# Performance work log

Hardware: AMD Instinct MI355X
Metric: run time of the kernel (lower is better)

## Reference

```python
import jax, jax.numpy as jnp
import numpy as np
import math

EMBED_DIM = 1024
NUM_HEADS = 16
HEAD_DIM = EMBED_DIM // NUM_HEADS
SEQ = 2048
BSZ = 2


def setup_inputs() -> dict:
    key = jax.random.key(0)
    ks = jax.random.split(key, 7)
    # xavier_uniform bound for in_proj_weight [3E, E]
    bound_in = math.sqrt(6.0 / (3 * EMBED_DIM + EMBED_DIM))
    bound_out = math.sqrt(1.0 / EMBED_DIM)  # nn.Linear default kaiming-ish bound
    return {
        "query": jax.random.normal(ks[0], (SEQ, BSZ, EMBED_DIM), dtype=jnp.float32),
        "key": jax.random.normal(ks[1], (SEQ, BSZ, EMBED_DIM), dtype=jnp.float32),
        "value": jax.random.normal(ks[2], (SEQ, BSZ, EMBED_DIM), dtype=jnp.float32),
        "in_proj_weight": jax.random.uniform(ks[3], (3 * EMBED_DIM, EMBED_DIM), minval=-bound_in, maxval=bound_in, dtype=jnp.float32),
        "in_proj_bias": jnp.zeros((3 * EMBED_DIM,), dtype=jnp.float32),
        "out_proj_weight": jax.random.uniform(ks[4], (EMBED_DIM, EMBED_DIM), minval=-bound_out, maxval=bound_out, dtype=jnp.float32),
        "out_proj_bias": jnp.zeros((EMBED_DIM,), dtype=jnp.float32),
    }


def reference(query, key, value, in_proj_weight, in_proj_bias, out_proj_weight, out_proj_bias):
    tgt_len, bsz, embed_dim = query.shape
    src_len = key.shape[0]
    h, d = NUM_HEADS, HEAD_DIM

    w_q, w_k, w_v = jnp.split(in_proj_weight, 3, axis=0)   # each [E, E]
    b_q, b_k, b_v = jnp.split(in_proj_bias, 3, axis=0)     # each [E]

    q = query @ w_q.T + b_q    # [T, B, E]
    k = key @ w_k.T + b_k      # [S, B, E]
    v = value @ w_v.T + b_v    # [S, B, E]

    # [T,B,E] -> [B, H, T, D]
    q = q.reshape(tgt_len, bsz, h, d).transpose(1, 2, 0, 3)
    k = k.reshape(src_len, bsz, h, d).transpose(1, 2, 0, 3)
    v = v.reshape(src_len, bsz, h, d).transpose(1, 2, 0, 3)

    scale = 1.0 / math.sqrt(d)
    scores = jnp.einsum("bhtd,bhsd->bhts", q, k) * scale   # [B, H, T, S]
    attn_probs = jax.nn.softmax(scores, axis=-1)
    out = jnp.einsum("bhts,bhsd->bhtd", attn_probs, v)      # [B, H, T, D]

    # [B,H,T,D] -> [T, B, E]
    out = out.transpose(2, 0, 1, 3).reshape(tgt_len, bsz, embed_dim)
    out = out @ out_proj_weight.T + out_proj_bias
    return (out, attn_probs)
```

## Files before the change

kernel.cpp:

```cpp
#include <hip/hip_runtime.h>


#define LDT 72

typedef __attribute__((ext_vector_type(8))) short short8;
typedef __attribute__((ext_vector_type(4))) float f32x4;

union V16 { float4 f4; unsigned long long u64[2]; unsigned short us[8]; };

__device__ inline unsigned short f2bf(float f) {
  union { float f; unsigned u; } v; v.f = f;
  unsigned u = v.u;
  u += 0x7FFFu + ((u >> 16) & 1u);
  return (unsigned short)(u >> 16);
}

__device__ inline short8 load8(const unsigned short* p) {
  union { short8 v; unsigned long long u[2]; } r;
  r.u[0] = *(const unsigned long long*)(p);
  r.u[1] = *(const unsigned long long*)(p + 4);
  return r.v;
}

__device__ inline void st16(unsigned short* dst, V16 v) {
  *(unsigned long long*)(dst) = v.u64[0];
  *(unsigned long long*)(dst + 4) = v.u64[1];
}

__global__ void cvt_bf16(const float* __restrict__ in, unsigned short* __restrict__ out, int n) {
  int i = (blockIdx.x * 256 + threadIdx.x) * 4;
  if (i < n) {
    float4 f = *(const float4*)(in + i);
    ushort4 o;
    o.x = f2bf(f.x); o.y = f2bf(f.y); o.z = f2bf(f.z); o.w = f2bf(f.w);
    *(ushort4*)(out + i) = o;
  }
}

__global__ __launch_bounds__(256, 2) void gemm_bt(
    const unsigned short* __restrict__ A,
    const unsigned short* __restrict__ Bw,
    const float* __restrict__ bias,
    void* __restrict__ Cv,
    int K, int ldc, int flags)
{
  __shared__ unsigned short As[128 * LDT];
  __shared__ unsigned short Bs[128 * LDT];
  int tid = threadIdx.x;
  int lane = tid & 63;
  int w = tid >> 6;
  int wm = (w & 1) * 64, wn = (w >> 1) * 64;
  int m0 = blockIdx.y * 128, n0 = blockIdx.x * 128;
  int quad = lane >> 4, c = lane & 15;

  f32x4 acc[4][4] = {};

  int lrow = tid >> 1;
  int lk = (tid & 1) * 32;
  const unsigned short* Ap = A + (size_t)(m0 + lrow) * K + lk;
  const unsigned short* Bp = Bw + (size_t)(n0 + lrow) * K + lk;
  unsigned short* AsW = As + lrow * LDT + lk;
  unsigned short* BsW = Bs + lrow * LDT + lk;

  for (int k0 = 0; k0 < K; k0 += 64) {
    V16 a0, a1, a2, a3, b0, b1, b2, b3;
    a0.f4 = *(const float4*)(Ap + k0);
    a1.f4 = *(const float4*)(Ap + k0 + 8);
    a2.f4 = *(const float4*)(Ap + k0 + 16);
    a3.f4 = *(const float4*)(Ap + k0 + 24);
    b0.f4 = *(const float4*)(Bp + k0);
    b1.f4 = *(const float4*)(Bp + k0 + 8);
    b2.f4 = *(const float4*)(Bp + k0 + 16);
    b3.f4 = *(const float4*)(Bp + k0 + 24);
    __syncthreads();
    st16(AsW, a0); st16(AsW + 8, a1); st16(AsW + 16, a2); st16(AsW + 24, a3);
    st16(BsW, b0); st16(BsW + 8, b1); st16(BsW + 16, b2); st16(BsW + 24, b3);
    __syncthreads();

    const unsigned short* Ab = As + (wm + c) * LDT + quad * 8;
    const unsigned short* Bb = Bs + (wn + c) * LDT + quad * 8;
#pragma unroll
    for (int ks = 0; ks < 2; ks++) {
      short8 af[4], bf[4];
#pragma unroll
      for (int i = 0; i < 4; i++) {
        af[i] = load8(Ab + i * 16 * LDT + ks * 32);
        bf[i] = load8(Bb + i * 16 * LDT + ks * 32);
      }
#pragma unroll
      for (int mi = 0; mi < 4; mi++)
#pragma unroll
        for (int ni = 0; ni < 4; ni++)
          acc[mi][ni] = __builtin_amdgcn_mfma_f32_16x16x32_bf16(af[mi], bf[ni], acc[mi][ni], 0, 0, 0);
    }
  }

#pragma unroll
  for (int mi = 0; mi < 4; mi++) {
#pragma unroll
    for (int ni = 0; ni < 4; ni++) {
      int col = n0 + wn + ni * 16 + c;
      float bv = bias[col];
#pragma unroll
      for (int r = 0; r < 4; r++) {
        int row = m0 + wm + mi * 16 + quad * 4 + r;
        float val = acc[mi][ni][r] + bv;
        if (flags & 2) val *= 0.125f;
        if (flags & 1) ((unsigned short*)Cv)[(size_t)row * ldc + col] = f2bf(val);
        else           ((float*)Cv)[(size_t)row * ldc + col] = val;
      }
    }
  }
}

__global__ __launch_bounds__(256, 2) void attn_fused(
    const unsigned short* __restrict__ QKV,
    float* __restrict__ probs,
    unsigned short* __restrict__ attnO)
{
  __shared__ unsigned short Qs[128 * LDT];
  __shared__ unsigned short Ks[64 * LDT];
  __shared__ unsigned short Ps[128 * LDT];
  __shared__ unsigned short Vts[64 * LDT];

  int tid = threadIdx.x, lane = tid & 63, w = tid >> 6;
  int bh = blockIdx.x >> 4;
  int tt = blockIdx.x & 15;
  int b = bh >> 4, h = bh & 15;
  int t0 = tt * 128;
  int quad = lane >> 4, c = lane & 15;
  int rbase = w * 32;

  {
    int row = tid >> 1, lk = (tid & 1) * 32;
    const unsigned short* src = QKV + ((size_t)((t0 + row) * 2 + b)) * 3072 + h * 64 + lk;
    V16 v0, v1, v2, v3;
    v0.f4 = *(const float4*)(src);
    v1.f4 = *(const float4*)(src + 8);
    v2.f4 = *(const float4*)(src + 16);
    v3.f4 = *(const float4*)(src + 24);
    unsigned short* dst = Qs + row * LDT + lk;
    st16(dst, v0); st16(dst + 8, v1); st16(dst + 16, v2); st16(dst + 24, v3);
  }

  int krow = tid >> 2, kseg = (tid & 3) * 16;
  const unsigned short* kbase = QKV + 1024 + h * 64 + kseg;
  const unsigned short* vbase = QKV + 2048 + h * 64 + kseg;
  unsigned short* ksdst = Ks + krow * LDT + kseg;

  float l_part[2][4] = {};

  for (int s0 = 0; s0 < 2048; s0 += 64) {
    V16 v0, v1;
    const unsigned short* src = kbase + ((size_t)((s0 + krow) * 2 + b)) * 3072;
    v0.f4 = *(const float4*)(src);
    v1.f4 = *(const float4*)(src + 8);
    __syncthreads();
    st16(ksdst, v0); st16(ksdst + 8, v1);
    __syncthreads();

    f32x4 sc[2][4] = {};
    const unsigned short* Ab = Qs + (rbase + c) * LDT + quad * 8;
    const unsigned short* Bb = Ks + c * LDT + quad * 8;
#pragma unroll
    for (int ks = 0; ks < 2; ks++) {
      short8 af[2], bfr[4];
      af[0] = load8(Ab + ks * 32);
      af[1] = load8(Ab + 16 * LDT + ks * 32);
#pragma unroll
      for (int ni = 0; ni < 4; ni++) bfr[ni] = load8(Bb + ni * 16 * LDT + ks * 32);
#pragma unroll
      for (int mi = 0; mi < 2; mi++)
#pragma unroll
        for (int ni = 0; ni < 4; ni++)
          sc[mi][ni] = __builtin_amdgcn_mfma_f32_16x16x32_bf16(af[mi], bfr[ni], sc[mi][ni], 0, 0, 0);
    }
#pragma unroll
    for (int mi = 0; mi < 2; mi++)
#pragma unroll
      for (int r = 0; r < 4; r++)
        l_part[mi][r] += __expf(sc[mi][0][r]) + __expf(sc[mi][1][r]) +
                         __expf(sc[mi][2][r]) + __expf(sc[mi][3][r]);
  }

  float rl[2][4];
#pragma unroll
  for (int mi = 0; mi < 2; mi++)
#pragma unroll
    for (int r = 0; r < 4; r++) {
      float s = l_part[mi][r];
      s += __shfl_xor(s, 1); s += __shfl_xor(s, 2);
      s += __shfl_xor(s, 4); s += __shfl_xor(s, 8);
      rl[mi][r] = 1.0f / s;
    }

  f32x4 acc_o[2][4] = {};
  size_t prow_base = ((size_t)bh * 2048 + t0) * 2048;

  for (int s0 = 0; s0 < 2048; s0 += 64) {
    V16 kv0, kv1, vv0, vv1;
    {
      const unsigned short* srcK = kbase + ((size_t)((s0 + krow) * 2 + b)) * 3072;
      kv0.f4 = *(const float4*)(srcK);
      kv1.f4 = *(const float4*)(srcK + 8);
      const unsigned short* srcV = vbase + ((size_t)((s0 + krow) * 2 + b)) * 3072;
      vv0.f4 = *(const float4*)(srcV);
      vv1.f4 = *(const float4*)(srcV + 8);
    }
    __syncthreads();
    st16(ksdst, kv0); st16(ksdst + 8, kv1);
#pragma unroll
    for (int j = 0; j < 8; j++) Vts[(kseg + j) * LDT + krow] = vv0.us[j];
#pragma unroll
    for (int j = 0; j < 8; j++) Vts[(kseg + 8 + j) * LDT + krow] = vv1.us[j];
    __syncthreads();

    f32x4 sc[2][4] = {};
    const unsigned short* Ab = Qs + (rbase + c) * LDT + quad * 8;
    const unsigned short* Bb = Ks + c * LDT + quad * 8;
#pragma unroll
    for (int ks = 0; ks < 2; ks++) {
      short8 af[2], bfr[4];
      af[0] = load8(Ab + ks * 32);
      af[1] = load8(Ab + 16 * LDT + ks * 32);
#pragma unroll
      for (int ni = 0; ni < 4; ni++) bfr[ni] = load8(Bb + ni * 16 * LDT + ks * 32);
#pragma unroll
      for (int mi = 0; mi < 2; mi++)
#pragma unroll
        for (int ni = 0; ni < 4; ni++)
          sc[mi][ni] = __builtin_amdgcn_mfma_f32_16x16x32_bf16(af[mi], bfr[ni], sc[mi][ni], 0, 0, 0);
    }

#pragma unroll
    for (int mi = 0; mi < 2; mi++)
#pragma unroll
      for (int ni = 0; ni < 4; ni++)
#pragma unroll
        for (int r = 0; r < 4; r++) {
          float p = __expf(sc[mi][ni][r]) * rl[mi][r];
          int rloc = rbase + mi * 16 + quad * 4 + r;
          int cloc = ni * 16 + c;
          probs[prow_base + (size_t)rloc * 2048 + s0 + cloc] = p;
          Ps[rloc * LDT + cloc] = f2bf(p);
        }
    __syncthreads();

    const unsigned short* Ab2 = Ps + (rbase + c) * LDT + quad * 8;
    const unsigned short* Bb2 = Vts + c * LDT + quad * 8;
#pragma unroll
    for (int ks = 0; ks < 2; ks++) {
      short8 af[2], bfr[4];
      af[0] = load8(Ab2 + ks * 32);
      af[1] = load8(Ab2 + 16 * LDT + ks * 32);
#pragma unroll
      for (int ni = 0; ni < 4; ni++) bfr[ni] = load8(Bb2 + ni * 16 * LDT + ks * 32);
#pragma unroll
      for (int mi = 0; mi < 2; mi++)
#pragma unroll
        for (int ni = 0; ni < 4; ni++)
          acc_o[mi][ni] = __builtin_amdgcn_mfma_f32_16x16x32_bf16(af[mi], bfr[ni], acc_o[mi][ni], 0, 0, 0);
    }
  }

#pragma unroll
  for (int mi = 0; mi < 2; mi++)
#pragma unroll
    for (int ni = 0; ni < 4; ni++)
#pragma unroll
      for (int r = 0; r < 4; r++) {
        int t = t0 + rbase + mi * 16 + quad * 4 + r;
        attnO[(size_t)(t * 2 + b) * 1024 + h * 64 + ni * 16 + c] = f2bf(acc_o[mi][ni][r]);
      }
}

extern "C" void kernel_launch(void* const* d_in, const int* in_sizes, int n_in,
                              void* d_out, int out_size, void* d_ws, size_t ws_size,
                              hipStream_t stream) {
  (void)in_sizes; (void)n_in; (void)out_size; (void)ws_size;
  const float* q_in  = (const float*)d_in[0];
  const float* k_in  = (const float*)d_in[1];
  const float* v_in  = (const float*)d_in[2];
  const float* w_in  = (const float*)d_in[3];
  const float* b_in  = (const float*)d_in[4];
  const float* w_out = (const float*)d_in[5];
  const float* b_out = (const float*)d_in[6];

  float* out0  = (float*)d_out;
  float* probs = out0 + (size_t)4096 * 1024;

  unsigned short* Xq  = (unsigned short*)d_ws;
  unsigned short* Xk  = Xq + (size_t)4096 * 1024;
  unsigned short* Xv  = Xk + (size_t)4096 * 1024;
  unsigned short* Wi  = Xv + (size_t)4096 * 1024;
  unsigned short* Wo  = Wi + (size_t)3072 * 1024;
  unsigned short* QKV = Wo + (size_t)1024 * 1024;
  unsigned short* AO  = QKV + (size_t)4096 * 3072;

  cvt_bf16<<<4096, 256, 0, stream>>>(q_in, Xq, 4194304);
  cvt_bf16<<<4096, 256, 0, stream>>>(k_in, Xk, 4194304);
  cvt_bf16<<<4096, 256, 0, stream>>>(v_in, Xv, 4194304);
  cvt_bf16<<<3072, 256, 0, stream>>>(w_in, Wi, 3145728);
  cvt_bf16<<<1024, 256, 0, stream>>>(w_out, Wo, 1048576);

  dim3 g1(8, 32);
  gemm_bt<<<g1, 256, 0, stream>>>(Xq, Wi,                       b_in,        QKV,        1024, 3072, 3);
  gemm_bt<<<g1, 256, 0, stream>>>(Xk, Wi + (size_t)1024 * 1024, b_in + 1024, QKV + 1024, 1024, 3072, 1);
  gemm_bt<<<g1, 256, 0, stream>>>(Xv, Wi + (size_t)2048 * 1024, b_in + 2048, QKV + 2048, 1024, 3072, 1);

  attn_fused<<<512, 256, 0, stream>>>(QKV, probs, AO);

  gemm_bt<<<g1, 256, 0, stream>>>(AO, Wo, b_out, (void*)out0, 1024, 1024, 0);
}
```

Baseline: 800.9 us.

## Use direct global-to-LDS loads, double-buffer K/V, pre-transpose V, merge launches

The GEMM and attention kernels now load tiles with global_load_lds into XOR-swizzled, unpadded shared memory. Attention double-buffers the K and V tiles, and V is transposed into a separate buffer by a new kernel so the in-loop scalar LDS transpose goes away. The five conversion launches become one, and the three QKV projections become a single 24x32-block launch. Probability stores switch to nontemporal, and the output projection uses a 64-wide N tile to get more blocks. The goal is lower load latency, fewer bank conflicts and less launch overhead, at the cost of an extra transpose pass and more LDS per block.

Measured after the change: 794.5 us. Within noise of the previous version (-0.8%).

```diff
diff --git a/kernel.cpp b/kernel.cpp
--- a/kernel.cpp
+++ b/kernel.cpp
@@ -8,98 +8,120 @@
 
 union V16 { float4 f4; unsigned long long u64[2]; unsigned short us[8]; };
 
-__device__ inline unsigned short f2bf(float f) {
+__device__ __forceinline__ unsigned short f2bf(float f) {
   union { float f; unsigned u; } v; v.f = f;
   unsigned u = v.u;
   u += 0x7FFFu + ((u >> 16) & 1u);
   return (unsigned short)(u >> 16);
 }
 
-__device__ inline short8 load8(const unsigned short* p) {
+__device__ __forceinline__ short8 load8(const unsigned short* p) {
   union { short8 v; unsigned long long u[2]; } r;
   r.u[0] = *(const unsigned long long*)(p);
   r.u[1] = *(const unsigned long long*)(p + 4);
   return r.v;
 }
 
-__device__ inline void st16(unsigned short* dst, V16 v) {
+__device__ __forceinline__ void st16(unsigned short* dst, V16 v) {
   *(unsigned long long*)(dst) = v.u64[0];
   *(unsigned long long*)(dst + 4) = v.u64[1];
 }
 
-__global__ void cvt_bf16(const float* __restrict__ in, unsigned short* __restrict__ out, int n) {
+typedef const __attribute__((address_space(1))) void* gas_t;
+typedef __attribute__((address_space(3))) void* las_t;
+__device__ __forceinline__ void gld16(const void* g, void* l) {
+  __builtin_amdgcn_global_load_lds((gas_t)g, (las_t)l, 16, 0, 0);
+}
+
+__global__ void cvt_all(const float* __restrict__ q, const float* __restrict__ k,
+                        const float* __restrict__ v, const float* __restrict__ wi,
+                        const float* __restrict__ wo,
+                        unsigned short* __restrict__ oq, unsigned short* __restrict__ ok2,
+                        unsigned short* __restrict__ ov, unsigned short* __restrict__ owi,
+                        unsigned short* __restrict__ owo) {
+  int y = blockIdx.y;
+  const float* src; unsigned short* dst; int n;
+  if (y == 0)      { src = q;  dst = oq;  n = 4194304; }
+  else if (y == 1) { src = k;  dst = ok2; n = 4194304; }
+  else if (y == 2) { src = v;  dst = ov;  n = 4194304; }
+  else if (y == 3) { src = wi; dst = owi; n = 3145728; }
+  else             { src = wo; dst = owo; n = 1048576; }
   int i = (blockIdx.x * 256 + threadIdx.x) * 4;
   if (i < n) {
-    float4 f = *(const float4*)(in + i);
+    float4 f = *(const float4*)(src + i);
     ushort4 o;
     o.x = f2bf(f.x); o.y = f2bf(f.y); o.z = f2bf(f.z); o.w = f2bf(f.w);
-    *(ushort4*)(out + i) = o;
-  }
-}
-
+    *(ushort4*)(dst + i) = o;
+  }
+}
+
+template<int BN>
 __global__ __launch_bounds__(256, 2) void gemm_bt(
-    const unsigned short* __restrict__ A,
-    const unsigned short* __restrict__ Bw,
+    const unsigned short* __restrict__ A0,
+    const unsigned short* __restrict__ A1,
+    const unsigned short* __restrict__ A2,
+    const unsigned short* __restrict__ W,
     const float* __restrict__ bias,
     void* __restrict__ Cv,
-    int K, int ldc, int flags)
+    int K, int ldc, int qkv)
 {
-  __shared__ unsigned short As[128 * LDT];
-  __shared__ unsigned short Bs[128 * LDT];
+  constexpr int NI = BN / 32;
+  __shared__ unsigned short As[128 * 64];
+  __shared__ unsigned short Bs[BN * 64];
   int tid = threadIdx.x;
   int lane = tid & 63;
   int w = tid >> 6;
-  int wm = (w & 1) * 64, wn = (w >> 1) * 64;
-  int m0 = blockIdx.y * 128, n0 = blockIdx.x * 128;
+  int wm = (w & 1) * 64, wn = (w >> 1) * (BN / 2);
+  int m0 = blockIdx.y * 128, n0g = blockIdx.x * BN;
+  int which = qkv ? (n0g >> 10) : 0;
+  const unsigned short* A = (which == 0) ? A0 : ((which == 1) ? A1 : A2);
+  const unsigned short* Bw = W + (size_t)which * (1u << 20);
+  int n0 = qkv ? (n0g & 1023) : n0g;
   int quad = lane >> 4, c = lane & 15;
-
-  f32x4 acc[4][4] = {};
-
-  int lrow = tid >> 1;
-  int lk = (tid & 1) * 32;
-  const unsigned short* Ap = A + (size_t)(m0 + lrow) * K + lk;
-  const unsigned short* Bp = Bw + (size_t)(n0 + lrow) * K + lk;
-  unsigned short* AsW = As + lrow * LDT + lk;
-  unsigned short* BsW = Bs + lrow * LDT + lk;
+  int sw8 = c & 7;
+
+  f32x4 acc[4][NI] = {};
+
+  int srow = lane >> 3;
+  int sseg = ((lane & 7) ^ srow) * 8;
+  const unsigned short* Asrc = A  + (size_t)(m0 + w * 32      + srow) * K + sseg;
+  const unsigned short* Bsrc = Bw + (size_t)(n0 + w * NI * 8  + srow) * K + sseg;
 
   for (int k0 = 0; k0 < K; k0 += 64) {
-    V16 a0, a1, a2, a3, b0, b1, b2, b3;
-    a0.f4 = *(const float4*)(Ap + k0);
-    a1.f4 = *(const float4*)(Ap + k0 + 8);
-    a2.f4 = *(const float4*)(Ap + k0 + 16);
-    a3.f4 = *(const float4*)(Ap + k0 + 24);
-    b0.f4 = *(const float4*)(Bp + k0);
-    b1.f4 = *(const float4*)(Bp + k0 + 8);
-    b2.f4 = *(const float4*)(Bp + k0 + 16);
-    b3.f4 = *(const float4*)(Bp + k0 + 24);
-    __syncthreads();
-    st16(AsW, a0); st16(AsW + 8, a1); st16(AsW + 16, a2); st16(AsW + 24, a3);
-    st16(BsW, b0); st16(BsW + 8, b1); st16(BsW + 16, b2); st16(BsW + 24, b3);
-    __syncthreads();
-
-    const unsigned short* Ab = As + (wm + c) * LDT + quad * 8;
-    const unsigned short* Bb = Bs + (wn + c) * LDT + quad * 8;
+    __syncthreads();
+#pragma unroll
+    for (int i = 0; i < 4; i++)
+      gld16(Asrc + (size_t)i * 8 * K + k0, As + (w * 32 + i * 8) * 64);
+#pragma unroll
+    for (int i = 0; i < NI; i++)
+      gld16(Bsrc + (size_t)i * 8 * K + k0, Bs + (w * NI * 8 + i * 8) * 64);
+    asm volatile("s_waitcnt vmcnt(0)" ::: "memory");
+    __syncthreads();
+
 #pragma unroll
     for (int ks = 0; ks < 2; ks++) {
-      short8 af[4], bf[4];
-#pragma unroll
-      for (int i = 0; i < 4; i++) {
-        af[i] = load8(Ab + i * 16 * LDT + ks * 32);
-        bf[i] = load8(Bb + i * 16 * LDT + ks * 32);
-      }
+      short8 af[4], bf_[NI];
+      int goff = ((quad | (ks << 2)) ^ sw8) * 8;
+#pragma unroll
+      for (int i = 0; i < 4; i++)
+        af[i] = load8(As + (wm + i * 16 + c) * 64 + goff);
+#pragma unroll
+      for (int ni = 0; ni < NI; ni++)
+        bf_[ni] = load8(Bs + (wn + ni * 16 + c) * 64 + goff);
 #pragma unroll
       for (int mi = 0; mi < 4; mi++)
 #pragma unroll
-        for (int ni = 0; ni < 4; ni++)
-          acc[mi][ni] = __builtin_amdgcn_mfma_f32_16x16x32_bf16(af[mi], bf[ni], acc[mi][ni], 0, 0, 0);
-    }
-  }
-
+        for (int ni = 0; ni < NI; ni++)
+          acc[mi][ni] = __builtin_amdgcn_mfma_f32_16x16x32_bf16(af[mi], bf_[ni], acc[mi][ni], 0, 0, 0);
+    }
+  }
+
+  int flags = qkv ? ((which == 0) ? 3 : 1) : 0;
 #pragma unroll
   for (int mi = 0; mi < 4; mi++) {
 #pragma unroll
-    for (int ni = 0; ni < 4; ni++) {
-      int col = n0 + wn + ni * 16 + c;
+    for (int ni = 0; ni < NI; ni++) {
+      int col = n0g + wn + ni * 16 + c;
       float bv = bias[col];
 #pragma unroll
       for (int r = 0; r < 4; r++) {
@@ -113,15 +135,44 @@
   }
 }
 
+__global__ __launch_bounds__(256) void transpose_v(const unsigned short* __restrict__ QKV,
+                                                   unsigned short* __restrict__ Vt) {
+  __shared__ unsigned short T[64 * 68];
+  int bh = blockIdx.y;
+  int b = bh >> 4, h = bh & 15;
+  int s0 = blockIdx.x * 64;
+  int t = threadIdx.x;
+  int sl = t >> 2, seg = (t & 3) * 16;
+  const unsigned short* src = QKV + ((size_t)((s0 + sl) * 2 + b)) * 3072 + 2048 + h * 64 + seg;
+  V16 a0, a1;
+  a0.f4 = *(const float4*)(src);
+  a1.f4 = *(const float4*)(src + 8);
+#pragma unroll
+  for (int j = 0; j < 8; j++) T[(seg + j) * 68 + sl] = a0.us[j];
+#pragma unroll
+  for (int j = 0; j < 8; j++) T[(seg + 8 + j) * 68 + sl] = a1.us[j];
+  __syncthreads();
+  int dl = t >> 2, s2 = (t & 3) * 16;
+  const unsigned short* tr = T + dl * 68 + s2;
+  V16 o0, o1;
+  o0.u64[0] = *(const unsigned long long*)(tr);
+  o0.u64[1] = *(const unsigned long long*)(tr + 4);
+  o1.u64[0] = *(const unsigned long long*)(tr + 8);
+  o1.u64[1] = *(const unsigned long long*)(tr + 12);
+  unsigned short* dst = Vt + ((size_t)bh * 64 + dl) * 2048 + s0 + s2;
+  st16(dst, o0); st16(dst + 8, o1);
+}
+
 __global__ __launch_bounds__(256, 2) void attn_fused(
     const unsigned short* __restrict__ QKV,
+    const unsigned short* __restrict__ Vt,
     float* __restrict__ probs,
     unsigned short* __restrict__ attnO)
 {
   __shared__ unsigned short Qs[128 * LDT];
-  __shared__ unsigned short Ks[64 * LDT];
+  __shared__ unsigned short Ks[2][64 * 64];
+  __shared__ unsigned short Vts[2][64 * 64];
   __shared__ unsigned short Ps[128 * LDT];
-  __shared__ unsigned short Vts[64 * LDT];
 
   int tid = threadIdx.x, lane = tid & 63, w = tid >> 6;
   int bh = blockIdx.x >> 4;
@@ -130,6 +181,7 @@
   int t0 = tt * 128;
   int quad = lane >> 4, c = lane & 15;
   int rbase = w * 32;
+  int sw8 = c & 7;
 
   {
     int row = tid >> 1, lk = (tid & 1) * 32;
@@ -143,32 +195,40 @@
     st16(dst, v0); st16(dst + 8, v1); st16(dst + 16, v2); st16(dst + 24, v3);
   }
 
-  int krow = tid >> 2, kseg = (tid & 3) * 16;
-  const unsigned short* kbase = QKV + 1024 + h * 64 + kseg;
-  const unsigned short* vbase = QKV + 2048 + h * 64 + kseg;
-  unsigned short* ksdst = Ks + krow * LDT + kseg;
+  int srow = lane >> 3;
+  int srs = ((lane & 7) ^ srow) * 8;
+  const unsigned short* Kbase = QKV + (size_t)b * 3072 + 1024 + h * 64 + srs + (size_t)srow * 6144;
+  const unsigned short* Vbase = Vt + ((size_t)bh * 64 + srow) * 2048 + srs;
 
   float l_part[2][4] = {};
 
+  int cur = 0;
+#pragma unroll
+  for (int i = 0; i < 2; i++)
+    gld16(Kbase + (size_t)(w * 16 + i * 8) * 6144, &Ks[0][(w * 16 + i * 8) * 64]);
+
   for (int s0 = 0; s0 < 2048; s0 += 64) {
-    V16 v0, v1;
-    const unsigned short* src = kbase + ((size_t)((s0 + krow) * 2 + b)) * 3072;
-    v0.f4 = *(const float4*)(src);
-    v1.f4 = *(const float4*)(src + 8);
-    __syncthreads();
-    st16(ksdst, v0); st16(ksdst + 8, v1);
-    __syncthreads();
+    asm volatile("s_waitcnt vmcnt(0)" ::: "memory");
+    __syncthreads();
+    if (s0 < 1984) {
+#pragma unroll
+      for (int i = 0; i < 2; i++)
+        gld16(Kbase + (size_t)(s0 + 64 + w * 16 + i * 8) * 6144,
+              &Ks[cur ^ 1][(w * 16 + i * 8) * 64]);
+    }
 
     f32x4 sc[2][4] = {};
     const unsigned short* Ab = Qs + (rbase + c) * LDT + quad * 8;
-    const unsigned short* Bb = Ks + c * LDT + quad * 8;
+    const unsigned short* Kc = Ks[cur];
 #pragma unroll
     for (int ks = 0; ks < 2; ks++) {
       short8 af[2], bfr[4];
       af[0] = load8(Ab + ks * 32);
       af[1] = load8(Ab + 16 * LDT + ks * 32);
-#pragma unroll
-      for (int ni = 0; ni < 4; ni++) bfr[ni] = load8(Bb + ni * 16 * LDT + ks * 32);
+      int goff = ((quad | (ks << 2)) ^ sw8) * 8;
+#pragma unroll
+      for (int ni = 0; ni < 4; ni++)
+        bfr[ni] = load8(Kc + (ni * 16 + c) * 64 + goff);
 #pragma unroll
       for (int mi = 0; mi < 2; mi++)
 #pragma unroll
@@ -181,6 +241,7 @@
       for (int r = 0; r < 4; r++)
         l_part[mi][r] += __expf(sc[mi][0][r]) + __expf(sc[mi][1][r]) +
                          __expf(sc[mi][2][r]) + __expf(sc[mi][3][r]);
+    cur ^= 1;
   }
 
   float rl[2][4];
@@ -197,34 +258,38 @@
   f32x4 acc_o[2][4] = {};
   size_t prow_base = ((size_t)bh * 2048 + t0) * 2048;
 
+  cur = 0;
+#pragma unroll
+  for (int i = 0; i < 2; i++) {
+    gld16(Kbase + (size_t)(w * 16 + i * 8) * 6144, &Ks[0][(w * 16 + i * 8) * 64]);
+    gld16(Vbase + (size_t)(w * 16 + i * 8) * 2048, &Vts[0][(w * 16 + i * 8) * 64]);
+  }
+
   for (int s0 = 0; s0 < 2048; s0 += 64) {
-    V16 kv0, kv1, vv0, vv1;
-    {
-      const unsigned short* srcK = kbase + ((size_t)((s0 + krow) * 2 + b)) * 3072;
-      kv0.f4 = *(const float4*)(srcK);
-      kv1.f4 = *(const float4*)(srcK + 8);
-      const unsigned short* srcV = vbase + ((size_t)((s0 + krow) * 2 + b)) * 3072;
-      vv0.f4 = *(const float4*)(srcV);
-      vv1.f4 = *(const float4*)(srcV + 8);
-    }
-    __syncthreads();
-    st16(ksdst, kv0); st16(ksdst + 8, kv1);
-#pragma unroll
-    for (int j = 0; j < 8; j++) Vts[(kseg + j) * LDT + krow] = vv0.us[j];
-#pragma unroll
-    for (int j = 0; j < 8; j++) Vts[(kseg + 8 + j) * LDT + krow] = vv1.us[j];
-    __syncthreads();
+    asm volatile("s_waitcnt vmcnt(0)" ::: "memory");
+    __syncthreads();
+    if (s0 < 1984) {
+#pragma unroll
+      for (int i = 0; i < 2; i++) {
+        gld16(Kbase + (size_t)(s0 + 64 + w * 16 + i * 8) * 6144,
+              &Ks[cur ^ 1][(w * 16 + i * 8) * 64]);
+        gld16(Vbase + (size_t)(w * 16 + i * 8) * 2048 + (s0 + 64),
+              &Vts[cur ^ 1][(w * 16 + i * 8) * 64]);
+      }
+    }
 
     f32x4 sc[2][4] = {};
     const unsigned short* Ab = Qs + (rbase + c) * LDT + quad * 8;
-    const unsigned short* Bb = Ks + c * LDT + quad * 8;
+    const unsigned short* Kc = Ks[cur];
 #pragma unroll
     for (int ks = 0; ks < 2; ks++) {
       short8 af[2], bfr[4];
       af[0] = load8(Ab + ks * 32);
       af[1] = load8(Ab + 16 * LDT + ks * 32);
-#pragma unroll
-      for (int ni = 0; ni < 4; ni++) bfr[ni] = load8(Bb + ni * 16 * LDT + ks * 32);
+      int goff = ((quad | (ks << 2)) ^ sw8) * 8;
+#pragma unroll
+      for (int ni = 0; ni < 4; ni++)
+        bfr[ni] = load8(Kc + (ni * 16 + c) * 64 + goff);
 #pragma unroll
       for (int mi = 0; mi < 2; mi++)
 #pragma unroll
@@ -235,32 +300,36 @@
 #pragma unroll
     for (int mi = 0; mi < 2; mi++)
 #pragma unroll
-      for (int ni = 0; ni < 4; ni++)
+      for (int ni = 0; ni < 4; ni++) {
+        int cloc = ni * 16 + c;
 #pragma unroll
         for (int r = 0; r < 4; r++) {
           float p = __expf(sc[mi][ni][r]) * rl[mi][r];
           int rloc = rbase + mi * 16 + quad * 4 + r;
-          int cloc = ni * 16 + c;
-          probs[prow_base + (size_t)rloc * 2048 + s0 + cloc] = p;
+          __builtin_nontemporal_store(p, probs + prow_base + (size_t)rloc * 2048 + s0 + cloc);
           Ps[rloc * LDT + cloc] = f2bf(p);
         }
+      }
     __syncthreads();
 
     const unsigned short* Ab2 = Ps + (rbase + c) * LDT + quad * 8;
-    const unsigned short* Bb2 = Vts + c * LDT + quad * 8;
+    const unsigned short* Vc = Vts[cur];
 #pragma unroll
     for (int ks = 0; ks < 2; ks++) {
       short8 af[2], bfr[4];
       af[0] = load8(Ab2 + ks * 32);
       af[1] = load8(Ab2 + 16 * LDT + ks * 32);
-#pragma unroll
-      for (int ni = 0; ni < 4; ni++) bfr[ni] = load8(Bb2 + ni * 16 * LDT + ks * 32);
+      int goff = ((quad | (ks << 2)) ^ sw8) * 8;
+#pragma unroll
+      for (int ni = 0; ni < 4; ni++)
+        bfr[ni] = load8(Vc + (ni * 16 + c) * 64 + goff);
 #pragma unroll
       for (int mi = 0; mi < 2; mi++)
 #pragma unroll
         for (int ni = 0; ni < 4; ni++)
           acc_o[mi][ni] = __builtin_amdgcn_mfma_f32_16x16x32_bf16(af[mi], bfr[ni], acc_o[mi][ni], 0, 0, 0);
     }
+    cur ^= 1;
   }
 
 #pragma unroll
@@ -296,19 +365,16 @@
   unsigned short* Wo  = Wi + (size_t)3072 * 1024;
   unsigned short* QKV = Wo + (size_t)1024 * 1024;
   unsigned short* AO  = QKV + (size_t)4096 * 3072;
-
-  cvt_bf16<<<4096, 256, 0, stream>>>(q_in, Xq, 4194304);
-  cvt_bf16<<<4096, 256, 0, stream>>>(k_in, Xk, 4194304);
-  cvt_bf16<<<4096, 256, 0, stream>>>(v_in, Xv, 4194304);
-  cvt_bf16<<<3072, 256, 0, stream>>>(w_in, Wi, 3145728);
-  cvt_bf16<<<1024, 256, 0, stream>>>(w_out, Wo, 1048576);
-
-  dim3 g1(8, 32);
-  gemm_bt<<<g1, 256, 0, stream>>>(Xq, Wi,                       b_in,        QKV,        1024, 3072, 3);
-  gemm_bt<<<g1, 256, 0, stream>>>(Xk, Wi + (size_t)1024 * 1024, b_in + 1024, QKV + 1024, 1024, 3072, 1);
-  gemm_bt<<<g1, 256, 0, stream>>>(Xv, Wi + (size_t)2048 * 1024, b_in + 2048, QKV + 2048, 1024, 3072, 1);
-
-  attn_fused<<<512, 256, 0, stream>>>(QKV, probs, AO);
-
-  gemm_bt<<<g1, 256, 0, stream>>>(AO, Wo, b_out, (void*)out0, 1024, 1024, 0);
-}
+  unsigned short* Vt  = AO + (size_t)4096 * 1024;
+
+  cvt_all<<<dim3(4096, 5), 256, 0, stream>>>(q_in, k_in, v_in, w_in, w_out,
+                                             Xq, Xk, Xv, Wi, Wo);
+
+  gemm_bt<128><<<dim3(24, 32), 256, 0, stream>>>(Xq, Xk, Xv, Wi, b_in, QKV, 1024, 3072, 1);
+
+  transpose_v<<<dim3(32, 32), 256, 0, stream>>>(QKV, Vt);
+
+  attn_fused<<<512, 256, 0, stream>>>(QKV, Vt, probs, AO);
+
+  gemm_bt<64><<<dim3(16, 32), 256, 0, stream>>>(AO, AO, AO, Wo, b_out, (void*)out0, 1024, 1024, 0);
+}
```
